# Performance work log

Measured on AMD Instinct MI355X. Metric: run time of the kernel, lower is better.

Reference implementation:

```python
import jax, jax.numpy as jnp
import numpy as np

N = 50000
E = 800000
F_IN = 128
HEADS = 4
OUT_PER_HEAD = 32  # out_features 128 / 4 heads
NEG_SLOPE = 0.2


def setup_inputs() -> dict:
    key = jax.random.key(0)
    k1, k2, k3, k4, k5 = jax.random.split(key, 5)
    x = jax.random.normal(k1, (N, F_IN), dtype=jnp.float32)
    edge_index = jax.random.randint(k2, (2, E), 0, N, dtype=jnp.int64)
    # xavier-uniform style init
    limW = float(np.sqrt(6.0 / (F_IN + OUT_PER_HEAD)))
    W = jax.random.uniform(k3, (HEADS, F_IN, OUT_PER_HEAD), jnp.float32, -limW, limW)
    lima = float(np.sqrt(6.0 / (OUT_PER_HEAD + 1)))
    a_l = jax.random.uniform(k4, (HEADS, OUT_PER_HEAD), jnp.float32, -lima, lima)
    a_r = jax.random.uniform(k5, (HEADS, OUT_PER_HEAD), jnp.float32, -lima, lima)
    return {"x": x, "edge_index": edge_index, "W": W, "a_l": a_l, "a_r": a_r}


def _leaky_relu(v, slope):
    return jnp.where(v >= 0, v, slope * v)


def reference(x, edge_index, W, a_l, a_r):
    src, dst = edge_index[0], edge_index[1]
    n = x.shape[0]
    # Wh: [heads, N, out_per_head]
    Wh = jnp.einsum('nf,kfh->knh', x, W)
    e_l = jnp.einsum('knh,kh->kn', Wh, a_l)  # [heads, N]
    e_r = jnp.einsum('knh,kh->kn', Wh, a_r)
    # per-edge attention logits [heads, E]
    e = _leaky_relu(e_l[:, src] + e_r[:, dst], NEG_SLOPE)
    # segment softmax over incoming edges of each dst node
    seg_max = jax.vmap(lambda ee: jax.ops.segment_max(ee, dst, num_segments=n))(e)
    seg_max = jnp.maximum(seg_max, -1e9)  # torch init value for empty nodes
    exp_e = jnp.exp(e - seg_max[:, dst])
    denom = jax.vmap(lambda ee: jax.ops.segment_sum(ee, dst, num_segments=n))(exp_e)
    alpha = exp_e / (denom[:, dst] + 1e-16)  # [heads, E]
    # weighted aggregation: [heads, E, out_per_head] scattered into [heads, N, out_per_head]
    weighted = alpha[..., None] * Wh[:, src, :]
    out = jax.vmap(lambda w: jax.ops.segment_sum(w, dst, num_segments=n))(weighted)
    # concat heads -> [N, heads*out_per_head]
    return out.transpose(1, 0, 2).reshape(n, -1)
```

## Files before the change

### kernel.cpp

```cpp
#include <hip/hip_runtime.h>

#define NN 50000
#define NE 800000
#define FIN 128
#define NH 4
#define OPH 32
#define FOUT 128
#define NSLOPE 0.2f
#define NGB ((NN + 63) / 64)
#define BCOLS 144
#define LDA 136
#define BSH 5
#define BUKSZ 32
#define NBUK ((NN + BUKSZ - 1) >> BSH)
#define CHUNK 8192
#define NPB1 ((NE + CHUNK - 1) / CHUNK)
#define SLOTP 32
#define SLOTQ 31
#define SLOTS 64
#define GRID1 (9 * NPB1)

typedef __attribute__((ext_vector_type(8))) short short8v;
typedef __attribute__((ext_vector_type(4))) float f32x4;

static __device__ __forceinline__ unsigned short f2bf(float f) {
  unsigned int u = __float_as_uint(f);
  u += 0x7fffu + ((u >> 16) & 1u);
  return (unsigned short)(u >> 16);
}

__global__ __launch_bounds__(128) void k_prep(
    const float* __restrict__ W, const float* __restrict__ a_l,
    const float* __restrict__ a_r, unsigned short* __restrict__ Btf) {
  const int c = blockIdx.x;
  const int f = threadIdx.x;
  unsigned short v = 0;
  if (c < 128) {
    const int h = c >> 5, o = c & 31;
    v = f2bf(W[h * (FIN * OPH) + f * OPH + o]);
  } else if (c < 136) {
    const int j = c - 128;
    const int h = j & 3;
    const float* __restrict__ av = (j < 4) ? a_l : a_r;
    float s = 0.f;
    for (int o = 0; o < 32; ++o)
      s += W[h * (FIN * OPH) + f * OPH + o] * av[h * OPH + o];
    v = f2bf(s);
  }
  const int ct = c >> 4, lr = c & 15;
  const int s = f >> 5, rem = f & 31, lk = rem >> 3, j = rem & 7;
  const int l = lr + 16 * lk;
  Btf[(((size_t)ct * 4 + s) * 64 + l) * 8 + j] = v;
}

__global__ __launch_bounds__(256) void k_gemm_part(
    const float* __restrict__ x, const unsigned short* __restrict__ Btf,
    const int* __restrict__ src, const int* __restrict__ dst,
    unsigned int* __restrict__ ebuf,
    unsigned short* __restrict__ WhU, float* __restrict__ e_l4,
    float* __restrict__ e_r4) {
  __shared__ union U {
    unsigned short As[64 * LDA];
    int cntl[NBUK];
  } sh;
  const int t = threadIdx.x;
  const int bid = blockIdx.x;

  if ((bid % 9) == 8) {
    const int part = bid / 9;
    const int base = part * CHUNK;
    for (int b = t; b < NBUK; b += 256) sh.cntl[b] = 0;
    __syncthreads();
    unsigned int* __restrict__ myreg = ebuf + (size_t)part * NBUK * SLOTP;
#pragma unroll
    for (int k = 0; k < CHUNK / 256; ++k) {
      const int i = base + k * 256 + t;
      if (i < NE) {
        const int d = dst[i];
        const unsigned int s = (unsigned int)src[i];
        const int b = d >> BSH;
        const int lp = atomicAdd(&sh.cntl[b], 1);
        if (lp < SLOTQ)
          myreg[b * SLOTP + 1 + lp] =
              ((unsigned int)(d & (BUKSZ - 1)) << 16) | s;
      }
    }
    __syncthreads();
    for (int b = t; b < NBUK; b += 256)
      myreg[b * SLOTP] = (unsigned int)min(sh.cntl[b], SLOTQ);
    return;
  }

  const int g = bid - (bid + 1) / 9;
  if (g >= NGB) return;
  const int m0 = g * 64;

#pragma unroll
  for (int i = 0; i < 8; ++i) {
    const int fidx = t + i * 256;
    const int node = fidx >> 5;
    const int fg = fidx & 31;
    const int n = m0 + node;
    float4 v = make_float4(0.f, 0.f, 0.f, 0.f);
    if (n < NN) v = *(const float4*)(x + (size_t)n * FIN + fg * 4);
    ushort4 pk;
    pk.x = f2bf(v.x); pk.y = f2bf(v.y); pk.z = f2bf(v.z); pk.w = f2bf(v.w);
    *(ushort4*)&sh.As[node * LDA + fg * 4] = pk;
  }
  __syncthreads();

  const int w = t >> 6;
  const int l = t & 63;
  const int lr = l & 15;
  const int lk = l >> 4;

  short8v a_frag[4];
#pragma unroll
  for (int kk = 0; kk < 4; ++kk)
    a_frag[kk] = *(const short8v*)&sh.As[(w * 16 + lr) * LDA + kk * 32 + lk * 8];

  f32x4 acc[9];
#pragma unroll
  for (int ct = 0; ct < 9; ++ct) acc[ct] = (f32x4){0.f, 0.f, 0.f, 0.f};

#pragma unroll
  for (int ct = 0; ct < 9; ++ct) {
    const unsigned short* __restrict__ Bp = Btf + ((size_t)ct * 4) * 512 + l * 8;
    short8v b0 = *(const short8v*)(Bp);
    short8v b1 = *(const short8v*)(Bp + 512);
    short8v b2 = *(const short8v*)(Bp + 1024);
    short8v b3 = *(const short8v*)(Bp + 1536);
    acc[ct] = __builtin_amdgcn_mfma_f32_16x16x32_bf16(a_frag[0], b0, acc[ct], 0, 0, 0);
    acc[ct] = __builtin_amdgcn_mfma_f32_16x16x32_bf16(a_frag[1], b1, acc[ct], 0, 0, 0);
    acc[ct] = __builtin_amdgcn_mfma_f32_16x16x32_bf16(a_frag[2], b2, acc[ct], 0, 0, 0);
    acc[ct] = __builtin_amdgcn_mfma_f32_16x16x32_bf16(a_frag[3], b3, acc[ct], 0, 0, 0);
  }

#pragma unroll
  for (int ct = 0; ct < 9; ++ct) {
#pragma unroll
    for (int reg = 0; reg < 4; ++reg) {
      const int n = m0 + w * 16 + lk * 4 + reg;
      if (n >= NN) continue;
      const float v = acc[ct][reg];
      if (ct < 8) {
        WhU[(size_t)n * FOUT + ct * 16 + lr] = f2bf(v);
      } else if (lr < 4) {
        e_l4[n * NH + lr] = v;
      } else if (lr < 8) {
        e_r4[n * NH + (lr - 4)] = v;
      }
    }
  }
}

__global__ __launch_bounds__(256) void k_lists_agg(
    const unsigned int* __restrict__ ebuf,
    const float* __restrict__ e_l4, const float* __restrict__ e_r4,
    const unsigned int* __restrict__ Whh, float* __restrict__ out) {
  __shared__ int lists[BUKSZ][SLOTS];
  __shared__ int cur[BUKSZ];
  __shared__ int pfx[128];
  __shared__ float exs[4][64][4];

  const int b = blockIdx.x;
  const int t = threadIdx.x;
  const int w = t >> 6;
  const int lane = t & 63;

  if (t < BUKSZ) cur[t] = 0;
  if (t < 128)
    pfx[t] = (t < NPB1)
                 ? (int)ebuf[((size_t)t * NBUK + b) * SLOTP]
                 : 0;
  __syncthreads();

  for (int d = 1; d < 128; d <<= 1) {
    int add = 0;
    if (t < 128 && t >= d) add = pfx[t - d];
    __syncthreads();
    if (t < 128) pfx[t] += add;
    __syncthreads();
  }
  const int T = pfx[127];

  for (int tid = t; tid < T; tid += 256) {
    int lo = 0, hi = 127;
    while (lo < hi) {
      const int mid = (lo + hi) >> 1;
      if (pfx[mid] > tid) hi = mid; else lo = mid + 1;
    }
    const int j = lo;
    const int p = tid - (j ? pfx[j - 1] : 0);
    const unsigned int v = ebuf[((size_t)j * NBUK + b) * SLOTP + 1 + p];
    const int idx = (int)(v >> 16);
    const int lp = atomicAdd(&cur[idx], 1);
    if (lp < SLOTS) lists[idx][lp] = (int)(v & 0xFFFFu);
  }
  __syncthreads();

  const int h = lane >> 4;
#pragma unroll
  for (int nl = 0; nl < 8; ++nl) {
    const int idx = w * 8 + nl;
    const int n = (b << BSH) + idx;
    if (n >= NN) continue;
    const int deg = min(cur[idx], SLOTS);
    const float4 ern = *(const float4*)&e_r4[n * NH];

    float e0 = 0.f, e1 = 0.f, e2 = 0.f, e3 = 0.f;
    if (lane < deg) {
      const int s = lists[idx][lane];
      const float4 el = *(const float4*)&e_l4[s * NH];
      float l0 = el.x + ern.x; l0 = (l0 >= 0.f) ? l0 : NSLOPE * l0;
      float l1 = el.y + ern.y; l1 = (l1 >= 0.f) ? l1 : NSLOPE * l1;
      float l2 = el.z + ern.z; l2 = (l2 >= 0.f) ? l2 : NSLOPE * l2;
      float l3 = el.w + ern.w; l3 = (l3 >= 0.f) ? l3 : NSLOPE * l3;
      e0 = __expf(l0); e1 = __expf(l1);
      e2 = __expf(l2); e3 = __expf(l3);
    }
    *(float4*)exs[w][lane] = make_float4(e0, e1, e2, e3);
    float D0 = e0, D1 = e1, D2 = e2, D3 = e3;
#pragma unroll
    for (int mm = 32; mm >= 1; mm >>= 1) {
      D0 += __shfl_xor(D0, mm);
      D1 += __shfl_xor(D1, mm);
      D2 += __shfl_xor(D2, mm);
      D3 += __shfl_xor(D3, mm);
    }

    float acc0 = 0.f, acc1 = 0.f;
    int jl = 0;
    for (; jl + 7 < deg; jl += 8) {
      int sj[8];
#pragma unroll
      for (int u = 0; u < 8; ++u) sj[u] = lists[idx][jl + u];
      unsigned int vv[8];
#pragma unroll
      for (int u = 0; u < 8; ++u) vv[u] = Whh[(size_t)sj[u] * 64 + lane];
#pragma unroll
      for (int u = 0; u < 8; ++u) {
        const float wH = exs[w][jl + u][h];
        acc0 = fmaf(wH, __uint_as_float(vv[u] << 16), acc0);
        acc1 = fmaf(wH, __uint_as_float(vv[u] & 0xffff0000u), acc1);
      }
    }
    for (; jl < deg; ++jl) {
      const int sj = lists[idx][jl];
      const float wH = exs[w][jl][h];
      const unsigned int v = Whh[(size_t)sj * 64 + lane];
      acc0 = fmaf(wH, __uint_as_float(v << 16), acc0);
      acc1 = fmaf(wH, __uint_as_float(v & 0xffff0000u), acc1);
    }

    const float dH = (h == 0) ? D0 : (h == 1) ? D1 : (h == 2) ? D2 : D3;
    const float inv = 1.f / (dH + 1e-16f);
    *(float2*)&out[(size_t)n * FOUT + 2 * lane] =
        make_float2(acc0 * inv, acc1 * inv);
  }
}

extern "C" void kernel_launch(void* const* d_in, const int* in_sizes, int n_in,
                              void* d_out, int out_size, void* d_ws, size_t ws_size,
                              hipStream_t stream) {
  const float* x   = (const float*)d_in[0];
  const int*   ei  = (const int*)d_in[1];
  const float* W   = (const float*)d_in[2];
  const float* a_l = (const float*)d_in[3];
  const float* a_r = (const float*)d_in[4];
  float* out = (float*)d_out;

  const int* src = ei;
  const int* dst = ei + NE;

  unsigned int* Whh = (unsigned int*)d_ws;
  float* e_l4     = (float*)(Whh + (size_t)NN * 64);
  float* e_r4     = e_l4 + NN * NH;
  unsigned short* Btf = (unsigned short*)(e_r4 + NN * NH);
  unsigned int* ebuf = (unsigned int*)(Btf + 9 * 4 * 64 * 8);
  (void)ws_size; (void)in_sizes; (void)n_in; (void)out_size;

  k_prep<<<BCOLS, 128, 0, stream>>>(W, a_l, a_r, Btf);

  k_gemm_part<<<GRID1, 256, 0, stream>>>(
      x, Btf, src, dst, ebuf, (unsigned short*)Whh, e_l4, e_r4);

  k_lists_agg<<<NBUK, 256, 0, stream>>>(ebuf, e_l4, e_r4, Whh, out);
}
```

Measured before the change: 80.04 us.

## Split edge bucketing blocks by bucket range to raise partition parallelism

Each edge-chunk partition block is now split into four blocks, each handling one quarter of the destination bucket range. Each block still reads the whole chunk's dst array but only bins edges whose bucket falls in its range. This shrinks shared-memory counters, cuts per-block atomic and store work, and raises the ratio of partition blocks to GEMM blocks in the interleaved grid from 1:8 to 1:2. The cost is four times the dst reads plus extra block launches.

```diff
diff --git a/kernel.cpp b/kernel.cpp
--- a/kernel.cpp
+++ b/kernel.cpp
@@ -15,10 +15,14 @@
 #define NBUK ((NN + BUKSZ - 1) >> BSH)
 #define CHUNK 8192
 #define NPB1 ((NE + CHUNK - 1) / CHUNK)
+#define RSPLIT 4
+#define RSPAN ((NBUK + RSPLIT - 1) / RSPLIT)
+#define NPARTB (NPB1 * RSPLIT)
 #define SLOTP 32
 #define SLOTQ 31
 #define SLOTS 64
-#define GRID1 (9 * NPB1)
+#define NTRIP 392
+#define GRID1 (3 * NTRIP)
 
 typedef __attribute__((ext_vector_type(8))) short short8v;
 typedef __attribute__((ext_vector_type(4))) float f32x4;
@@ -61,15 +65,19 @@
     float* __restrict__ e_r4) {
   __shared__ union U {
     unsigned short As[64 * LDA];
-    int cntl[NBUK];
+    int cntl[RSPAN + 1];
   } sh;
   const int t = threadIdx.x;
   const int bid = blockIdx.x;
 
-  if ((bid % 9) == 8) {
-    const int part = bid / 9;
+  if (bid % 3 == 2) {
+    const int pidx = bid / 3;
+    const int part = pidx >> 2;
+    const int r = pidx & 3;
+    const int lob = r * RSPAN;
+    const int hib = min(lob + RSPAN, NBUK);
     const int base = part * CHUNK;
-    for (int b = t; b < NBUK; b += 256) sh.cntl[b] = 0;
+    for (int b = t; b < RSPAN; b += 256) sh.cntl[b] = 0;
     __syncthreads();
     unsigned int* __restrict__ myreg = ebuf + (size_t)part * NBUK * SLOTP;
 #pragma unroll
@@ -77,21 +85,22 @@
       const int i = base + k * 256 + t;
       if (i < NE) {
         const int d = dst[i];
-        const unsigned int s = (unsigned int)src[i];
         const int b = d >> BSH;
-        const int lp = atomicAdd(&sh.cntl[b], 1);
-        if (lp < SLOTQ)
-          myreg[b * SLOTP + 1 + lp] =
-              ((unsigned int)(d & (BUKSZ - 1)) << 16) | s;
+        if (b >= lob && b < hib) {
+          const int lp = atomicAdd(&sh.cntl[b - lob], 1);
+          if (lp < SLOTQ)
+            myreg[b * SLOTP + 1 + lp] =
+                ((unsigned int)(d & (BUKSZ - 1)) << 16) | (unsigned int)src[i];
+        }
       }
     }
     __syncthreads();
-    for (int b = t; b < NBUK; b += 256)
-      myreg[b * SLOTP] = (unsigned int)min(sh.cntl[b], SLOTQ);
+    for (int b = lob + t; b < hib; b += 256)
+      myreg[b * SLOTP] = (unsigned int)min(sh.cntl[b - lob], SLOTQ);
     return;
   }
 
-  const int g = bid - (bid + 1) / 9;
+  const int g = (bid / 3) * 2 + (bid % 3);
   if (g >= NGB) return;
   const int m0 = g * 64;
 
```

Measured after the change: 80.40 us. Within noise of the previous version (+0.4%).
